# Optimization experiments

Hardware: AMD Instinct MI355X
Metric: run time of the kernel (lower is better)

## Reference

```python
import jax, jax.numpy as jnp
import numpy as np

LN_EPS = 1e-5

def setup_inputs() -> dict:
    key = jax.random.key(0)
    ks = jax.random.split(key, 12)
    B, T, R, Ds = 4, 128, 64, 128
    N = 2048
    d_id = 128
    max_neurons, max_regions, max_eids = 2048, 128, 256
    U = jax.random.normal(ks[0], (B, T, R, Ds), dtype=jnp.float32)
    neuron_regions = jax.random.randint(ks[1], (B, N), 0, max_regions, dtype=jnp.int32)
    eids = jax.random.randint(ks[2], (B,), 0, max_eids, dtype=jnp.int32)
    r_map = jax.random.randint(ks[3], (max_regions,), 0, R, dtype=jnp.int32)
    s = 0.02
    neuron_slot = jax.random.normal(ks[4], (max_neurons, d_id), dtype=jnp.float32) * s
    region_emb = jax.random.normal(ks[5], (max_regions, d_id), dtype=jnp.float32) * s
    eid_emb = jax.random.normal(ks[6], (max_eids, d_id), dtype=jnp.float32) * s
    ln_gamma = jnp.ones((d_id,), dtype=jnp.float32)
    ln_beta = jnp.zeros((d_id,), dtype=jnp.float32)
    W1 = jax.random.normal(ks[7], (d_id, 2 * Ds), dtype=jnp.float32) * (1.0 / np.sqrt(d_id))
    b1 = jnp.zeros((2 * Ds,), dtype=jnp.float32)
    W2 = jax.random.normal(ks[8], (2 * Ds, Ds + 1), dtype=jnp.float32) * (1.0 / np.sqrt(2 * Ds))
    b2 = jnp.zeros((Ds + 1,), dtype=jnp.float32)  # nn.init.zeros_ on hyper[-1].bias
    return {"U": U, "neuron_regions": neuron_regions, "eids": eids, "r_map": r_map,
            "neuron_slot": neuron_slot, "region_emb": region_emb, "eid_emb": eid_emb,
            "ln_gamma": ln_gamma, "ln_beta": ln_beta, "W1": W1, "b1": b1, "W2": W2, "b2": b2}


def reference(U, neuron_regions, eids, r_map, neuron_slot, region_emb, eid_emb,
              ln_gamma, ln_beta, W1, b1, W2, b2):
    B, T, R, Ds = U.shape
    N = neuron_regions.shape[1]
    # neuron identity embedding: slot + region (+ eid)
    nr = jnp.clip(neuron_regions, 0, region_emb.shape[0] - 1)
    e = neuron_slot[:N][None, :, :] + region_emb[nr]                      # [B,N,d_id]
    e = e + eid_emb[jnp.clip(eids, 0, eid_emb.shape[0] - 1)][:, None, :]
    # hyper-MLP: LayerNorm -> Linear -> GELU(exact) -> Linear
    mu = e.mean(-1, keepdims=True)
    var = ((e - mu) ** 2).mean(-1, keepdims=True)
    h = (e - mu) * jax.lax.rsqrt(var + LN_EPS) * ln_gamma + ln_beta
    h = jax.nn.gelu(h @ W1 + b1, approximate=False)
    wb = h @ W2 + b2                                                      # [B,N,Ds+1]
    w = wb[..., :Ds]                                                      # [B,N,Ds]
    bias = wb[..., Ds]                                                    # [B,N]
    # region-indexed gather + weighted reduce
    local_r = r_map[jnp.clip(neuron_regions, 0, r_map.shape[0] - 1)]      # [B,N]
    lr_safe = jnp.clip(local_r, 0, None)
    idx = jnp.broadcast_to(lr_safe[:, None, :, None], (B, T, N, Ds))
    U_neur = jnp.take_along_axis(U, idx, axis=2)                          # [B,T,N,Ds]
    pred = jnp.einsum('btnd,bnd->btn', U_neur, w) + bias[:, None, :]
    pred = jnp.where((local_r < 0)[:, None, :], jnp.zeros_like(pred), pred)
    return pred
```

## Files before the change

kernel.cpp:

```cpp
#include <hip/hip_runtime.h>
#include <hip/hip_bf16.h>
#include <math.h>

#define DEV __device__ __forceinline__

typedef __attribute__((ext_vector_type(8))) short short8v;
typedef __attribute__((ext_vector_type(4))) float f32x4;

DEV float bf2f(unsigned short u) { return __uint_as_float(((unsigned)u) << 16); }
DEV unsigned short f2bf(float x) {
    unsigned u = __float_as_uint(x);
    return (unsigned short)((u + 0x7fffu + ((u >> 16) & 1u)) >> 16);
}
DEV unsigned pack2(float lo, float hi) {
    return ((unsigned)f2bf(hi) << 16) | (unsigned)f2bf(lo);
}
DEV f32x4 mfma16(short8v a, short8v b, f32x4 c) {
    return __builtin_amdgcn_mfma_f32_16x16x32_bf16(a, b, c, 0, 0, 0);
}

DEV float gelu_fast(float x) {
    const float z  = x * 0.70710678118654752f;
    const float az = fabsf(z);
    const float t  = __builtin_amdgcn_rcpf(fmaf(0.3275911f, az, 1.0f));
    float p = fmaf(t, 1.061405429f, -1.453152027f);
    p = fmaf(t, p, 1.421413741f);
    p = fmaf(t, p, -0.284496736f);
    p = fmaf(t, p, 0.254829592f);
    p = p * t;
    const float E = __builtin_amdgcn_exp2f(z * z * -1.4426950408889634f);
    const float erf_az = fmaf(-p, E, 1.0f);
    const float erf_z  = copysignf(erf_az, z);
    const float hx = 0.5f * x;
    return fmaf(hx, erf_z, hx);
}

#define NN 2048

__global__ __launch_bounds__(256, 1) void prep_kernel(
    const float* __restrict__ W1, const float* __restrict__ W2,
    const int* __restrict__ r_map, const int* __restrict__ neuron_regions,
    unsigned short* __restrict__ W1T, unsigned short* __restrict__ W2T,
    float* __restrict__ w2col, int* __restrict__ order, int* __restrict__ offs)
{
    __shared__ __align__(16) float T[32][33];
    __shared__ int hist[65], starts[66], cursor[65];
    const int tid = threadIdx.x;
    const int bid = blockIdx.x;

    if (bid < 32) {
        const int tr = bid >> 3, tc = bid & 7;
#pragma unroll
        for (int p = 0; p < 4; p++) {
            const int i = p * 8 + (tid >> 5), j = tid & 31;
            T[i][j] = W1[(tr * 32 + i) * 256 + tc * 32 + j];
        }
        __syncthreads();
#pragma unroll
        for (int p = 0; p < 4; p++) {
            const int i = p * 8 + (tid >> 5), j = tid & 31;
            W1T[(tc * 32 + i) * 128 + tr * 32 + j] = f2bf(T[j][i]);
        }
    } else if (bid < 64) {
        const int bb = bid - 32, tr = bb >> 2, tc = bb & 3;
#pragma unroll
        for (int p = 0; p < 4; p++) {
            const int i = p * 8 + (tid >> 5), j = tid & 31;
            T[i][j] = W2[(tr * 32 + i) * 129 + tc * 32 + j];
        }
        __syncthreads();
#pragma unroll
        for (int p = 0; p < 4; p++) {
            const int i = p * 8 + (tid >> 5), j = tid & 31;
            W2T[(tc * 32 + i) * 256 + tr * 32 + j] = f2bf(T[j][i]);
        }
    } else if (bid == 64) {
        w2col[tid] = W2[tid * 129 + 128];
    } else {
        const int b = bid - 65;
        for (int i = tid; i < 65; i += 256) hist[i] = 0;
        __syncthreads();
        for (int n = tid; n < NN; n += 256) {
            int nr = min(max(neuron_regions[b * NN + n], 0), 127);
            int lr = r_map[nr];
            int bin = (lr < 0) ? 64 : min(lr, 63);
            atomicAdd(&hist[bin], 1);
        }
        __syncthreads();
        if (tid == 0) {
            int run = 0;
            for (int i = 0; i < 65; i++) { starts[i] = run; cursor[i] = run; run += hist[i]; }
            starts[65] = run;
        }
        __syncthreads();
        for (int i = tid; i < 66; i += 256) offs[b * 66 + i] = starts[i];
        for (int n = tid; n < NN; n += 256) {
            int nr = min(max(neuron_regions[b * NN + n], 0), 127);
            int lr = r_map[nr];
            int bin = (lr < 0) ? 64 : min(lr, 63);
            int pos = atomicAdd(&cursor[bin], 1);
            order[b * NN + pos] = n;
        }
    }
}

__global__ __launch_bounds__(256, 1) void p1_kernel(
    const int* __restrict__ neuron_regions, const int* __restrict__ eids,
    const float* __restrict__ neuron_slot, const float* __restrict__ region_emb,
    const float* __restrict__ eid_emb, const float* __restrict__ ln_gamma,
    const float* __restrict__ ln_beta, const float* __restrict__ b1,
    const float* __restrict__ b2, const unsigned short* __restrict__ W1T,
    const unsigned short* __restrict__ W2T, const float* __restrict__ w2col,
    unsigned short* __restrict__ w_ws, float* __restrict__ bias_ws)
{
    __shared__ __align__(16) unsigned short hT[16][136];
    __shared__ __align__(16) unsigned short H1[16][264];
    __shared__ float biasp[16];
    const int tid = threadIdx.x;
    const int row0 = blockIdx.x * 16;
    if (tid < 16) biasp[tid] = 0.f;

    {
        const int rr = tid >> 4, q = tid & 15;
        const int row = row0 + rr;
        const int b = row >> 11, n = row & (NN - 1);
        int nr = min(max(neuron_regions[b * NN + n], 0), 127);
        int eid = min(max(eids[b], 0), 255);
        const float* ns = neuron_slot + n * 128 + q * 8;
        const float* re = region_emb + nr * 128 + q * 8;
        const float* ee = eid_emb + eid * 128 + q * 8;
        float e[8];
        {
            float4 a0 = *(const float4*)ns, a1 = *(const float4*)(ns + 4);
            float4 c0 = *(const float4*)re, c1 = *(const float4*)(re + 4);
            float4 d0 = *(const float4*)ee, d1 = *(const float4*)(ee + 4);
            e[0] = a0.x + c0.x + d0.x; e[1] = a0.y + c0.y + d0.y;
            e[2] = a0.z + c0.z + d0.z; e[3] = a0.w + c0.w + d0.w;
            e[4] = a1.x + c1.x + d1.x; e[5] = a1.y + c1.y + d1.y;
            e[6] = a1.z + c1.z + d1.z; e[7] = a1.w + c1.w + d1.w;
        }
        float s = 0.f, s2 = 0.f;
#pragma unroll
        for (int i = 0; i < 8; i++) { s += e[i]; s2 += e[i] * e[i]; }
        s += __shfl_xor(s, 1);  s2 += __shfl_xor(s2, 1);
        s += __shfl_xor(s, 2);  s2 += __shfl_xor(s2, 2);
        s += __shfl_xor(s, 4);  s2 += __shfl_xor(s2, 4);
        s += __shfl_xor(s, 8);  s2 += __shfl_xor(s2, 8);
        const float mu = s * (1.f / 128.f);
        const float var = s2 * (1.f / 128.f) - mu * mu;
        const float rstd = rsqrtf(var + 1e-5f);
        float4 g0 = *(const float4*)(ln_gamma + q * 8), g1 = *(const float4*)(ln_gamma + q * 8 + 4);
        float4 t0 = *(const float4*)(ln_beta + q * 8),  t1 = *(const float4*)(ln_beta + q * 8 + 4);
        float gm[8] = {g0.x, g0.y, g0.z, g0.w, g1.x, g1.y, g1.z, g1.w};
        float bt[8] = {t0.x, t0.y, t0.z, t0.w, t1.x, t1.y, t1.z, t1.w};
        float h[8];
#pragma unroll
        for (int i = 0; i < 8; i++) h[i] = (e[i] - mu) * rstd * gm[i] + bt[i];
        uint4 pk;
        pk.x = pack2(h[0], h[1]); pk.y = pack2(h[2], h[3]);
        pk.z = pack2(h[4], h[5]); pk.w = pack2(h[6], h[7]);
        *(uint4*)&hT[rr][q * 8] = pk;
    }
    __syncthreads();

    const int wv = tid >> 6, l = tid & 63;
    const int lr = l & 15, lh = l >> 4;

    short8v afr[4];
#pragma unroll
    for (int ks = 0; ks < 4; ks++)
        afr[ks] = *(const short8v*)&hT[lr][ks * 32 + lh * 8];

    f32x4 acc1[4];
    short8v bfr[4][4];
    float w2c[4];
#pragma unroll
    for (int nt = 0; nt < 4; nt++) {
        const int n = wv * 64 + nt * 16 + lr;
#pragma unroll
        for (int ks = 0; ks < 4; ks++)
            bfr[nt][ks] = *(const short8v*)(W1T + n * 128 + ks * 32 + lh * 8);
        const float bb = b1[n];
        acc1[nt].x = bb; acc1[nt].y = bb; acc1[nt].z = bb; acc1[nt].w = bb;
        w2c[nt] = w2col[n];
    }
#pragma unroll
    for (int nt = 0; nt < 4; nt++)
#pragma unroll
        for (int ks = 0; ks < 4; ks++)
            acc1[nt] = mfma16(afr[ks], bfr[nt][ks], acc1[nt]);

    float pb[4] = {0.f, 0.f, 0.f, 0.f};
#pragma unroll
    for (int nt = 0; nt < 4; nt++) {
        const int n = wv * 64 + nt * 16 + lr;
#pragma unroll
        for (int j = 0; j < 4; j++) {
            const float g = gelu_fast(acc1[nt][j]);
            H1[lh * 4 + j][n] = f2bf(g);
            pb[j] += g * w2c[nt];
        }
    }
#pragma unroll
    for (int j = 0; j < 4; j++) {
        pb[j] += __shfl_xor(pb[j], 1);
        pb[j] += __shfl_xor(pb[j], 2);
        pb[j] += __shfl_xor(pb[j], 4);
        pb[j] += __shfl_xor(pb[j], 8);
    }
    if (lr == 0) {
#pragma unroll
        for (int j = 0; j < 4; j++) atomicAdd(&biasp[lh * 4 + j], pb[j]);
    }
    __syncthreads();

    if (tid < 16) bias_ws[row0 + tid] = biasp[tid] + b2[128];

    short8v a2[8];
#pragma unroll
    for (int ks = 0; ks < 8; ks++)
        a2[ks] = *(const short8v*)&H1[lr][ks * 32 + lh * 8];

    f32x4 acc2[2];
    short8v b2f[2][8];
#pragma unroll
    for (int nt = 0; nt < 2; nt++) {
        const int n = wv * 32 + nt * 16 + lr;
#pragma unroll
        for (int ks = 0; ks < 8; ks++)
            b2f[nt][ks] = *(const short8v*)(W2T + n * 256 + ks * 32 + lh * 8);
        const float bb = b2[n];
        acc2[nt].x = bb; acc2[nt].y = bb; acc2[nt].z = bb; acc2[nt].w = bb;
    }
#pragma unroll
    for (int nt = 0; nt < 2; nt++)
#pragma unroll
        for (int ks = 0; ks < 8; ks++)
            acc2[nt] = mfma16(a2[ks], b2f[nt][ks], acc2[nt]);

#pragma unroll
    for (int nt = 0; nt < 2; nt++) {
        const int n = wv * 32 + nt * 16 + lr;
#pragma unroll
        for (int j = 0; j < 4; j++)
            hT[lh * 4 + j][n] = f2bf(acc2[nt][j]);
    }
    __syncthreads();
    {
        const int r = tid >> 4, c = tid & 15;
        uint4 v = *(const uint4*)&hT[r][c * 8];
        *(uint4*)(w_ws + (row0 + r) * 128 + c * 8) = v;
    }
}

__global__ __launch_bounds__(256, 1) void p2_kernel(
    const float* __restrict__ U, const int* __restrict__ order,
    const int* __restrict__ offs, const unsigned short* __restrict__ w_ws,
    const float* __restrict__ bias_ws, float* __restrict__ out)
{
    __shared__ __align__(16) unsigned short Ubf[128][136];
    __shared__ __align__(16) unsigned short Bt[32][136];
    __shared__ int nidS[32];
    __shared__ float biasS[32];
    const int tid = threadIdx.x;
    const int bid = blockIdx.x;

    if (bid >= 256) {
        const int b = bid - 256;
        const int s64 = offs[b * 66 + 64], s65 = offs[b * 66 + 65];
        const int cnt = s65 - s64;
        for (int idx = tid; idx < cnt * 128; idx += 256) {
            const int j = idx >> 7, t = idx & 127;
            const int n = order[b * NN + s64 + j];
            out[(b * 128 + t) * NN + n] = 0.f;
        }
        return;
    }

    const int b = bid >> 6, slot = bid & 63;
    const int s0 = offs[b * 66 + slot], s1 = offs[b * 66 + slot + 1];
    const int cnt = s1 - s0;
    if (cnt <= 0) return;

    {
        const int t = tid >> 1, half = tid & 1;
        const float* src = U + ((size_t)((b * 128 + t) * 64 + slot)) * 128 + half * 64;
        unsigned short* dst = &Ubf[t][half * 64];
#pragma unroll
        for (int j = 0; j < 16; j++) {
            float4 v = ((const float4*)src)[j];
            ((uint2*)dst)[j] = make_uint2(pack2(v.x, v.y), pack2(v.z, v.w));
        }
    }
    __syncthreads();

    const int wv = tid >> 6, l = tid & 63;
    const int lr = l & 15, lh = l >> 4;

    short8v afr[2][4];
#pragma unroll
    for (int mt = 0; mt < 2; mt++)
#pragma unroll
        for (int ks = 0; ks < 4; ks++)
            afr[mt][ks] = *(const short8v*)&Ubf[wv * 32 + mt * 16 + lr][ks * 32 + lh * 8];

    const int nChunks = (cnt + 31) >> 5;
    for (int c = 0; c < nChunks; c++) {
        const int base = s0 + c * 32;
        const int cc = min(cnt - c * 32, 32);
        __syncthreads();
        if (tid < 32) {
            const int nid = (tid < cc) ? order[b * NN + base + tid] : -1;
            nidS[tid] = nid;
            biasS[tid] = (nid >= 0) ? bias_ws[b * NN + nid] : 0.f;
        }
        {
            const int jj = tid >> 3, q = tid & 7;
            const int nid = (jj < cc) ? order[b * NN + base + jj] : -1;
            unsigned short* dst = &Bt[jj][q * 16];
            if (nid >= 0) {
                const uint4* src = (const uint4*)(w_ws + ((size_t)(b * NN + nid)) * 128 + q * 16);
                ((uint4*)dst)[0] = src[0];
                ((uint4*)dst)[1] = src[1];
            } else {
                ((uint4*)dst)[0] = make_uint4(0, 0, 0, 0);
                ((uint4*)dst)[1] = make_uint4(0, 0, 0, 0);
            }
        }
        __syncthreads();

        f32x4 acc[2][2];
#pragma unroll
        for (int mt = 0; mt < 2; mt++)
#pragma unroll
            for (int nt = 0; nt < 2; nt++) {
                acc[mt][nt].x = 0.f; acc[mt][nt].y = 0.f;
                acc[mt][nt].z = 0.f; acc[mt][nt].w = 0.f;
            }
        short8v bfr[2][4];
#pragma unroll
        for (int nt = 0; nt < 2; nt++)
#pragma unroll
            for (int ks = 0; ks < 4; ks++)
                bfr[nt][ks] = *(const short8v*)&Bt[nt * 16 + lr][ks * 32 + lh * 8];
#pragma unroll
        for (int mt = 0; mt < 2; mt++)
#pragma unroll
            for (int nt = 0; nt < 2; nt++)
#pragma unroll
                for (int ks = 0; ks < 4; ks++)
                    acc[mt][nt] = mfma16(afr[mt][ks], bfr[nt][ks], acc[mt][nt]);

#pragma unroll
        for (int nt = 0; nt < 2; nt++) {
            const int j = nt * 16 + lr;
            const int nid = nidS[j];
            if (nid >= 0) {
                const float bs = biasS[j];
#pragma unroll
                for (int mt = 0; mt < 2; mt++) {
                    const int tt = wv * 32 + mt * 16 + lh * 4;
#pragma unroll
                    for (int jr = 0; jr < 4; jr++)
                        out[(b * 128 + tt + jr) * NN + nid] = acc[mt][nt][jr] + bs;
                }
            }
        }
    }
}

extern "C" void kernel_launch(void* const* d_in, const int* in_sizes, int n_in,
                              void* d_out, int out_size, void* d_ws, size_t ws_size,
                              hipStream_t stream)
{
    const float* U              = (const float*)d_in[0];
    const int*   neuron_regions = (const int*)d_in[1];
    const int*   eids           = (const int*)d_in[2];
    const int*   r_map          = (const int*)d_in[3];
    const float* neuron_slot    = (const float*)d_in[4];
    const float* region_emb     = (const float*)d_in[5];
    const float* eid_emb        = (const float*)d_in[6];
    const float* ln_gamma       = (const float*)d_in[7];
    const float* ln_beta        = (const float*)d_in[8];
    const float* W1             = (const float*)d_in[9];
    const float* b1             = (const float*)d_in[10];
    const float* W2             = (const float*)d_in[11];
    const float* b2             = (const float*)d_in[12];

    char* ws = (char*)d_ws;
    unsigned short* w_ws  = (unsigned short*)(ws);
    float*          bias_ws = (float*)(ws + 2097152);
    unsigned short* W1T   = (unsigned short*)(ws + 2129920);
    unsigned short* W2T   = (unsigned short*)(ws + 2195456);
    float*          w2col = (float*)(ws + 2260992);
    int*            order = (int*)(ws + 2262016);
    int*            offs  = (int*)(ws + 2294784);
    float* outp = (float*)d_out;

    hipLaunchKernelGGL(prep_kernel, dim3(69), dim3(256), 0, stream,
                       W1, W2, r_map, neuron_regions, W1T, W2T, w2col, order, offs);
    hipLaunchKernelGGL(p1_kernel, dim3(512), dim3(256), 0, stream,
                       neuron_regions, eids, neuron_slot, region_emb, eid_emb,
                       ln_gamma, ln_beta, b1, b2, W1T, W2T, w2col, w_ws, bias_ws);
    hipLaunchKernelGGL(p2_kernel, dim3(260), dim3(256), 0, stream,
                       U, order, offs, w_ws, bias_ws, outp);
}
```

Baseline: 40.35 us.

## Split p2 work into per-chunk blocks via descriptor list and half time tiles

The prep kernel now builds a per-batch list of (region slot, 32-neuron chunk) descriptors, and p2 launches one block per descriptor and per half of the time axis instead of one block per region looping over chunks. This addresses load imbalance and the low block count in p2, where regions with many neurons serialized their chunks. In exchange, each U row slice is re-read and converted once per chunk instead of once per region. p1 and p2 also interleave MFMA with the B-fragment loads and raise launch_bounds occupancy hints to cut register pressure. Finally, a __syncthreads is added before hT is reused in p1.

Measured after the change: 49.43 us. 1.23x slower.

```diff
diff --git a/kernel.cpp b/kernel.cpp
--- a/kernel.cpp
+++ b/kernel.cpp
@@ -7,7 +7,6 @@
 typedef __attribute__((ext_vector_type(8))) short short8v;
 typedef __attribute__((ext_vector_type(4))) float f32x4;
 
-DEV float bf2f(unsigned short u) { return __uint_as_float(((unsigned)u) << 16); }
 DEV unsigned short f2bf(float x) {
     unsigned u = __float_as_uint(x);
     return (unsigned short)((u + 0x7fffu + ((u >> 16) & 1u)) >> 16);
@@ -41,7 +40,8 @@
     const float* __restrict__ W1, const float* __restrict__ W2,
     const int* __restrict__ r_map, const int* __restrict__ neuron_regions,
     unsigned short* __restrict__ W1T, unsigned short* __restrict__ W2T,
-    float* __restrict__ w2col, int* __restrict__ order, int* __restrict__ offs)
+    float* __restrict__ w2col, int* __restrict__ order, int* __restrict__ offs,
+    int* __restrict__ desc, int* __restrict__ dcount)
 {
     __shared__ __align__(16) float T[32][33];
     __shared__ int hist[65], starts[66], cursor[65];
@@ -91,6 +91,13 @@
             int run = 0;
             for (int i = 0; i < 65; i++) { starts[i] = run; cursor[i] = run; run += hist[i]; }
             starts[65] = run;
+            int k = 0;
+            for (int s2 = 0; s2 < 64; s2++) {
+                const int len = starts[s2 + 1] - starts[s2];
+                for (int base = 0; base < len; base += 32)
+                    desc[b * 128 + k++] = s2 | (base << 8);
+            }
+            dcount[b] = k;
         }
         __syncthreads();
         for (int i = tid; i < 66; i += 256) offs[b * 66 + i] = starts[i];
@@ -104,7 +111,7 @@
     }
 }
 
-__global__ __launch_bounds__(256, 1) void p1_kernel(
+__global__ __launch_bounds__(256, 2) void p1_kernel(
     const int* __restrict__ neuron_regions, const int* __restrict__ eids,
     const float* __restrict__ neuron_slot, const float* __restrict__ region_emb,
     const float* __restrict__ eid_emb, const float* __restrict__ ln_gamma,
@@ -172,23 +179,21 @@
         afr[ks] = *(const short8v*)&hT[lr][ks * 32 + lh * 8];
 
     f32x4 acc1[4];
-    short8v bfr[4][4];
     float w2c[4];
 #pragma unroll
     for (int nt = 0; nt < 4; nt++) {
         const int n = wv * 64 + nt * 16 + lr;
+        short8v bfr[4];
 #pragma unroll
         for (int ks = 0; ks < 4; ks++)
-            bfr[nt][ks] = *(const short8v*)(W1T + n * 128 + ks * 32 + lh * 8);
+            bfr[ks] = *(const short8v*)(W1T + n * 128 + ks * 32 + lh * 8);
         const float bb = b1[n];
-        acc1[nt].x = bb; acc1[nt].y = bb; acc1[nt].z = bb; acc1[nt].w = bb;
+        f32x4 a; a.x = bb; a.y = bb; a.z = bb; a.w = bb;
+#pragma unroll
+        for (int ks = 0; ks < 4; ks++) a = mfma16(afr[ks], bfr[ks], a);
+        acc1[nt] = a;
         w2c[nt] = w2col[n];
     }
-#pragma unroll
-    for (int nt = 0; nt < 4; nt++)
-#pragma unroll
-        for (int ks = 0; ks < 4; ks++)
-            acc1[nt] = mfma16(afr[ks], bfr[nt][ks], acc1[nt]);
 
     float pb[4] = {0.f, 0.f, 0.f, 0.f};
 #pragma unroll
@@ -222,22 +227,21 @@
         a2[ks] = *(const short8v*)&H1[lr][ks * 32 + lh * 8];
 
     f32x4 acc2[2];
-    short8v b2f[2][8];
 #pragma unroll
     for (int nt = 0; nt < 2; nt++) {
         const int n = wv * 32 + nt * 16 + lr;
+        short8v bf[8];
 #pragma unroll
         for (int ks = 0; ks < 8; ks++)
-            b2f[nt][ks] = *(const short8v*)(W2T + n * 256 + ks * 32 + lh * 8);
+            bf[ks] = *(const short8v*)(W2T + n * 256 + ks * 32 + lh * 8);
         const float bb = b2[n];
-        acc2[nt].x = bb; acc2[nt].y = bb; acc2[nt].z = bb; acc2[nt].w = bb;
-    }
-#pragma unroll
-    for (int nt = 0; nt < 2; nt++)
-#pragma unroll
-        for (int ks = 0; ks < 8; ks++)
-            acc2[nt] = mfma16(a2[ks], b2f[nt][ks], acc2[nt]);
-
+        f32x4 a; a.x = bb; a.y = bb; a.z = bb; a.w = bb;
+#pragma unroll
+        for (int ks = 0; ks < 8; ks++) a = mfma16(a2[ks], bf[ks], a);
+        acc2[nt] = a;
+    }
+
+    __syncthreads();
 #pragma unroll
     for (int nt = 0; nt < 2; nt++) {
         const int n = wv * 32 + nt * 16 + lr;
@@ -253,118 +257,99 @@
     }
 }
 
-__global__ __launch_bounds__(256, 1) void p2_kernel(
+__global__ __launch_bounds__(256, 3) void p2_kernel(
     const float* __restrict__ U, const int* __restrict__ order,
-    const int* __restrict__ offs, const unsigned short* __restrict__ w_ws,
+    const int* __restrict__ offs, const int* __restrict__ desc,
+    const int* __restrict__ dcount, const unsigned short* __restrict__ w_ws,
     const float* __restrict__ bias_ws, float* __restrict__ out)
 {
-    __shared__ __align__(16) unsigned short Ubf[128][136];
+    __shared__ __align__(16) unsigned short Ubf[64][136];
     __shared__ __align__(16) unsigned short Bt[32][136];
     __shared__ int nidS[32];
     __shared__ float biasS[32];
     const int tid = threadIdx.x;
     const int bid = blockIdx.x;
-
-    if (bid >= 256) {
-        const int b = bid - 256;
-        const int s64 = offs[b * 66 + 64], s65 = offs[b * 66 + 65];
-        const int cnt = s65 - s64;
-        for (int idx = tid; idx < cnt * 128; idx += 256) {
-            const int j = idx >> 7, t = idx & 127;
-            const int n = order[b * NN + s64 + j];
-            out[(b * 128 + t) * NN + n] = 0.f;
+    const int bb = bid >> 8, thalf = (bid >> 7) & 1, ci = bid & 127;
+    const int t0 = thalf * 64;
+
+    const int dcnt = dcount[bb];
+    if (ci > dcnt) return;
+    if (ci == dcnt) {
+        const int d0 = offs[bb * 66 + 64];
+        const int dc = offs[bb * 66 + 65] - d0;
+        for (int idx = tid; idx < dc * 64; idx += 256) {
+            const int j = idx >> 6, t = idx & 63;
+            out[(size_t)(bb * 128 + t0 + t) * NN + order[bb * NN + d0 + j]] = 0.f;
         }
         return;
     }
 
-    const int b = bid >> 6, slot = bid & 63;
-    const int s0 = offs[b * 66 + slot], s1 = offs[b * 66 + slot + 1];
-    const int cnt = s1 - s0;
-    if (cnt <= 0) return;
+    const int d = desc[bb * 128 + ci];
+    const int slot = d & 63;
+    const int base = d >> 8;
+    const int s0 = offs[bb * 66 + slot];
+    const int cnt = offs[bb * 66 + slot + 1] - s0;
+    const int cc = min(cnt - base, 32);
 
     {
-        const int t = tid >> 1, half = tid & 1;
-        const float* src = U + ((size_t)((b * 128 + t) * 64 + slot)) * 128 + half * 64;
-        unsigned short* dst = &Ubf[t][half * 64];
-#pragma unroll
-        for (int j = 0; j < 16; j++) {
+        const int t = tid >> 2, q = tid & 3;
+        const float* src = U + ((size_t)((bb * 128 + t0 + t) * 64 + slot)) * 128 + q * 32;
+        unsigned short* dst = &Ubf[t][q * 32];
+#pragma unroll
+        for (int j = 0; j < 8; j++) {
             float4 v = ((const float4*)src)[j];
             ((uint2*)dst)[j] = make_uint2(pack2(v.x, v.y), pack2(v.z, v.w));
         }
     }
+
+    if (tid < 32) {
+        const int nid = (tid < cc) ? order[bb * NN + s0 + base + tid] : -1;
+        nidS[tid] = nid;
+        biasS[tid] = (nid >= 0) ? bias_ws[bb * NN + nid] : 0.f;
+    }
+    {
+        const int jj = tid >> 3, q = tid & 7;
+        const int nid = (jj < cc) ? order[bb * NN + s0 + base + jj] : -1;
+        unsigned short* dst = &Bt[jj][q * 16];
+        if (nid >= 0) {
+            const uint4* src = (const uint4*)(w_ws + ((size_t)(bb * NN + nid)) * 128 + q * 16);
+            ((uint4*)dst)[0] = src[0];
+            ((uint4*)dst)[1] = src[1];
+        } else {
+            ((uint4*)dst)[0] = make_uint4(0, 0, 0, 0);
+            ((uint4*)dst)[1] = make_uint4(0, 0, 0, 0);
+        }
+    }
     __syncthreads();
 
     const int wv = tid >> 6, l = tid & 63;
     const int lr = l & 15, lh = l >> 4;
 
-    short8v afr[2][4];
-#pragma unroll
-    for (int mt = 0; mt < 2; mt++)
+    short8v afr[4];
+#pragma unroll
+    for (int ks = 0; ks < 4; ks++)
+        afr[ks] = *(const short8v*)&Ubf[wv * 16 + lr][ks * 32 + lh * 8];
+
+    short8v bfr[2][4];
+#pragma unroll
+    for (int nt = 0; nt < 2; nt++)
 #pragma unroll
         for (int ks = 0; ks < 4; ks++)
-            afr[mt][ks] = *(const short8v*)&Ubf[wv * 32 + mt * 16 + lr][ks * 32 + lh * 8];
-
-    const int nChunks = (cnt + 31) >> 5;
-    for (int c = 0; c < nChunks; c++) {
-        const int base = s0 + c * 32;
-        const int cc = min(cnt - c * 32, 32);
-        __syncthreads();
-        if (tid < 32) {
-            const int nid = (tid < cc) ? order[b * NN + base + tid] : -1;
-            nidS[tid] = nid;
-            biasS[tid] = (nid >= 0) ? bias_ws[b * NN + nid] : 0.f;
-        }
-        {
-            const int jj = tid >> 3, q = tid & 7;
-            const int nid = (jj < cc) ? order[b * NN + base + jj] : -1;
-            unsigned short* dst = &Bt[jj][q * 16];
-            if (nid >= 0) {
-                const uint4* src = (const uint4*)(w_ws + ((size_t)(b * NN + nid)) * 128 + q * 16);
-                ((uint4*)dst)[0] = src[0];
-                ((uint4*)dst)[1] = src[1];
-            } else {
-                ((uint4*)dst)[0] = make_uint4(0, 0, 0, 0);
-                ((uint4*)dst)[1] = make_uint4(0, 0, 0, 0);
-            }
-        }
-        __syncthreads();
-
-        f32x4 acc[2][2];
-#pragma unroll
-        for (int mt = 0; mt < 2; mt++)
-#pragma unroll
-            for (int nt = 0; nt < 2; nt++) {
-                acc[mt][nt].x = 0.f; acc[mt][nt].y = 0.f;
-                acc[mt][nt].z = 0.f; acc[mt][nt].w = 0.f;
-            }
-        short8v bfr[2][4];
-#pragma unroll
-        for (int nt = 0; nt < 2; nt++)
-#pragma unroll
-            for (int ks = 0; ks < 4; ks++)
-                bfr[nt][ks] = *(const short8v*)&Bt[nt * 16 + lr][ks * 32 + lh * 8];
-#pragma unroll
-        for (int mt = 0; mt < 2; mt++)
-#pragma unroll
-            for (int nt = 0; nt < 2; nt++)
-#pragma unroll
-                for (int ks = 0; ks < 4; ks++)
-                    acc[mt][nt] = mfma16(afr[mt][ks], bfr[nt][ks], acc[mt][nt]);
-
-#pragma unroll
-        for (int nt = 0; nt < 2; nt++) {
-            const int j = nt * 16 + lr;
-            const int nid = nidS[j];
-            if (nid >= 0) {
-                const float bs = biasS[j];
-#pragma unroll
-                for (int mt = 0; mt < 2; mt++) {
-                    const int tt = wv * 32 + mt * 16 + lh * 4;
-#pragma unroll
-                    for (int jr = 0; jr < 4; jr++)
-                        out[(b * 128 + tt + jr) * NN + nid] = acc[mt][nt][jr] + bs;
-                }
-            }
+            bfr[nt][ks] = *(const short8v*)&Bt[nt * 16 + lr][ks * 32 + lh * 8];
+
+#pragma unroll
+    for (int nt = 0; nt < 2; nt++) {
+        f32x4 a; a.x = 0.f; a.y = 0.f; a.z = 0.f; a.w = 0.f;
+#pragma unroll
+        for (int ks = 0; ks < 4; ks++) a = mfma16(afr[ks], bfr[nt][ks], a);
+        const int j = nt * 16 + lr;
+        const int nid = nidS[j];
+        if (nid >= 0) {
+            const float bs = biasS[j];
+#pragma unroll
+            for (int jr = 0; jr < 4; jr++)
+                out[(size_t)(bb * 128 + t0 + wv * 16 + lh * 4 + jr) * NN + nid] =
+                    a[jr] + bs;
         }
     }
 }
@@ -388,20 +373,23 @@
     const float* b2             = (const float*)d_in[12];
 
     char* ws = (char*)d_ws;
-    unsigned short* w_ws  = (unsigned short*)(ws);
-    float*          bias_ws = (float*)(ws + 2097152);
-    unsigned short* W1T   = (unsigned short*)(ws + 2129920);
-    unsigned short* W2T   = (unsigned short*)(ws + 2195456);
-    float*          w2col = (float*)(ws + 2260992);
-    int*            order = (int*)(ws + 2262016);
-    int*            offs  = (int*)(ws + 2294784);
+    unsigned short* w_ws    = (unsigned short*)(ws);
+    float*          bias_ws = (float*)(ws + 0x200000);
+    unsigned short* W1T     = (unsigned short*)(ws + 0x208000);
+    unsigned short* W2T     = (unsigned short*)(ws + 0x218000);
+    float*          w2col   = (float*)(ws + 0x228000);
+    int*            order   = (int*)(ws + 0x229000);
+    int*            offs    = (int*)(ws + 0x231000);
+    int*            desc    = (int*)(ws + 0x232000);
+    int*            dcount  = (int*)(ws + 0x232800);
     float* outp = (float*)d_out;
 
     hipLaunchKernelGGL(prep_kernel, dim3(69), dim3(256), 0, stream,
-                       W1, W2, r_map, neuron_regions, W1T, W2T, w2col, order, offs);
+                       W1, W2, r_map, neuron_regions, W1T, W2T, w2col,
+                       order, offs, desc, dcount);
     hipLaunchKernelGGL(p1_kernel, dim3(512), dim3(256), 0, stream,
                        neuron_regions, eids, neuron_slot, region_emb, eid_emb,
                        ln_gamma, ln_beta, b1, b2, W1T, W2T, w2col, w_ws, bias_ws);
-    hipLaunchKernelGGL(p2_kernel, dim3(260), dim3(256), 0, stream,
-                       U, order, offs, w_ws, bias_ws, outp);
-}
+    hipLaunchKernelGGL(p2_kernel, dim3(1024), dim3(256), 0, stream,
+                       U, order, offs, desc, dcount, w_ws, bias_ws, outp);
+}
```
